# Kernel tuning notes

Measured on AMD Instinct MI355X. Metric: run time of the kernel, lower is better.

The kernel has to match this reference:

```python
import jax, jax.numpy as jnp
import numpy as np

B, T, C, H = 8, 1024, 768, 12
HD = C // H  # 64

def setup_inputs() -> dict:
    key = jax.random.key(0)
    ks = jax.random.split(key, 5)
    s = 0.02
    return {
        "x": jax.random.normal(ks[0], (B, T, C), dtype=jnp.float32),
        "w_attn": jax.random.normal(ks[1], (C, 3 * C), dtype=jnp.float32) * s,
        "b_attn": jnp.zeros((3 * C,), dtype=jnp.float32),
        "w_proj": jax.random.normal(ks[2], (C, C), dtype=jnp.float32) * s,
        "b_proj": jnp.zeros((C,), dtype=jnp.float32),
    }

def reference(x, w_attn, b_attn, w_proj, b_proj):
    Bx, Tx, Cx = x.shape
    qkv = x @ w_attn + b_attn                      # [B,T,3C]
    q, k, v = jnp.split(qkv, 3, axis=-1)
    # [B,H,T,hd]
    q = q.reshape(Bx, Tx, H, HD).transpose(0, 2, 1, 3)
    k = k.reshape(Bx, Tx, H, HD).transpose(0, 2, 1, 3)
    v = v.reshape(Bx, Tx, H, HD).transpose(0, 2, 1, 3)
    scale = 1.0 / jnp.sqrt(jnp.asarray(HD, dtype=x.dtype))
    scores = jnp.einsum('bhqd,bhkd->bhqk', q, k) * scale  # [B,H,T,T]
    causal = jnp.tril(jnp.ones((Tx, Tx), dtype=bool))
    scores = jnp.where(causal, scores, jnp.asarray(-jnp.inf, dtype=x.dtype))
    weights = jax.nn.softmax(scores, axis=-1)
    y = jnp.einsum('bhqk,bhkd->bhqd', weights, v)  # [B,H,T,hd]
    y = y.transpose(0, 2, 1, 3).reshape(Bx, Tx, Cx)
    return y @ w_proj + b_proj
```

## Files before the change

kernel.cpp:

```cpp
#include <hip/hip_runtime.h>
#include <cstdint>
#include <cstddef>

#define B_  8
#define T_  1024
#define C_  768
#define H_  12
#define HD_ 64
#define K3_ 2304

typedef unsigned short u16;
typedef __attribute__((ext_vector_type(8))) short bf16x8;
typedef __attribute__((ext_vector_type(4))) float f32x4;

#define MFMA __builtin_amdgcn_mfma_f32_16x16x32_bf16

__device__ __forceinline__ u16 f2bf(float f) {
    unsigned u = __builtin_bit_cast(unsigned, f);
    u += 0x7fffu + ((u >> 16) & 1u);
    return (u16)(u >> 16);
}

__device__ __forceinline__ unsigned pk2bf(float a, float b) {
    unsigned ua = __builtin_bit_cast(unsigned, a) + 0x8000u;
    unsigned ub = __builtin_bit_cast(unsigned, b) + 0x8000u;
    return (ua >> 16) | (ub & 0xffff0000u);
}

#define GLL16(gp, lp) __builtin_amdgcn_global_load_lds( \
    (__attribute__((address_space(1))) unsigned int*)(gp), \
    (__attribute__((address_space(3))) unsigned int*)(lp), 16, 0, 0)

__device__ __forceinline__ void tcvt_tile(const float* __restrict__ in, u16* __restrict__ out,
                                          int R, int Cc, int bx, int by, int tid, float* tile ) {
    int bc = bx * 32, br = by * 32;
    int tx = tid & 31, ty = tid >> 5;
    #pragma unroll
    for (int kk = 0; kk < 32; kk += 8)
        tile[(ty + kk) * 33 + tx] = in[(size_t)(br + ty + kk) * Cc + bc + tx];
    __syncthreads();
    #pragma unroll
    for (int kk = 0; kk < 32; kk += 8)
        out[(size_t)(bc + ty + kk) * R + br + tx] = f2bf(tile[tx * 33 + ty + kk]);
}

__global__ void prep(const float* __restrict__ x, u16* __restrict__ xb,
                     const float* __restrict__ wa, u16* __restrict__ wat,
                     const float* __restrict__ wp, u16* __restrict__ wpt) {
    __shared__ float tile[32 * 33];
    int bid = blockIdx.x, tid = threadIdx.x;
    if (bid < 6144) {
        int i = bid * 256 + tid;
        float4 v = ((const float4*)x)[i];
        ushort4 o;
        o.x = f2bf(v.x); o.y = f2bf(v.y); o.z = f2bf(v.z); o.w = f2bf(v.w);
        ((ushort4*)xb)[i] = o;
    } else if (bid < 6144 + 1728) {
        int b = bid - 6144;
        tcvt_tile(wa, wat, C_, K3_, b % 72, b / 72, tid, tile);
    } else {
        int b = bid - 7872;
        tcvt_tile(wp, wpt, C_, C_, b % 24, b / 24, tid, tile);
    }
}

__launch_bounds__(256)
__global__ void gemm_qkv(const u16* __restrict__ A, const u16* __restrict__ Bt,
                         const float* __restrict__ bias,
                         u16* __restrict__ q, u16* __restrict__ k, u16* __restrict__ v) {
    const int K = C_;
    __shared__ __align__(16) u16 SM[16896];
    u16 (*As)[64] = (u16(*)[64])SM;
    u16 (*Bs)[64] = (u16(*)[64])(SM + 8192);
    u16 (*Cs)[132] = (u16(*)[132])SM;
    int tid = threadIdx.x;
    int id = blockIdx.x;
    int xcd = id & 7, jj = id >> 3;
    int m0 = (xcd * 8 + (jj & 7)) * 128;
    int n0 = (jj >> 3) * 128;
    int lane = tid & 63, wv = tid >> 6;
    int wm = (wv >> 1) * 64, wn = (wv & 1) * 64;
    int r16 = lane & 15, quad = lane >> 4;

    f32x4 acc[4][4] = {};
    int srow = tid >> 3;
    int gblk = (tid & 7) ^ (srow & 7);
    const u16* Ag = A  + (size_t)(m0 + srow) * K + gblk * 8;
    const u16* Bg = Bt + (size_t)(n0 + srow) * K + gblk * 8;
    u16* Al = SM + tid * 8;
    u16* Bl = SM + 8192 + tid * 8;
    int sw = r16 & 7;

    for (int kt = 0; kt < K; kt += 64) {
        #pragma unroll
        for (int s = 0; s < 4; s++) {
            GLL16(Ag + (size_t)(s * 32) * K + kt, Al + s * 2048);
            GLL16(Bg + (size_t)(s * 32) * K + kt, Bl + s * 2048);
        }
        __syncthreads();
        #pragma unroll
        for (int kk = 0; kk < 2; kk++) {
            bf16x8 af[4], bfr[4];
            #pragma unroll
            for (int i = 0; i < 4; i++) af[i]  = *(const bf16x8*)&As[wm + i * 16 + r16][((kk * 4 + quad) ^ sw) * 8];
            #pragma unroll
            for (int j = 0; j < 4; j++) bfr[j] = *(const bf16x8*)&Bs[wn + j * 16 + r16][((kk * 4 + quad) ^ sw) * 8];
            #pragma unroll
            for (int i = 0; i < 4; i++)
                #pragma unroll
                for (int j = 0; j < 4; j++)
                    acc[i][j] = MFMA(af[i], bfr[j], acc[i][j], 0, 0, 0);
        }
        __syncthreads();
    }

    int sec = n0 / C_;
    int cc0 = n0 - sec * C_;
    int b = m0 >> 10, t0 = m0 & 1023;

    if (sec == 2) {
        #pragma unroll
        for (int i = 0; i < 4; i++) {
            #pragma unroll
            for (int j = 0; j < 4; j++) {
                int cc = cc0 + wn + j * 16 + r16;
                float bv = bias[2 * C_ + cc];
                int h = cc >> 6, hd = cc & 63;
                int t = t0 + wm + i * 16 + quad * 4;
                ushort4 ov;
                ov.x = f2bf(acc[i][j][0] + bv); ov.y = f2bf(acc[i][j][1] + bv);
                ov.z = f2bf(acc[i][j][2] + bv); ov.w = f2bf(acc[i][j][3] + bv);
                *(ushort4*)(v + (((size_t)b * H_ + h) * HD_ + hd) * T_ + t) = ov;
            }
        }
    } else {
        float scale = (sec == 0) ? 0.125f : 1.0f;
        u16* dst = (sec == 0) ? q : k;
        #pragma unroll
        for (int i = 0; i < 4; i++)
            #pragma unroll
            for (int j = 0; j < 4; j++) {
                int col = wn + j * 16 + r16;
                float bv = bias[sec * C_ + cc0 + col];
                #pragma unroll
                for (int r = 0; r < 4; r++)
                    Cs[wm + i * 16 + quad * 4 + r][col] = f2bf((acc[i][j][r] + bv) * scale);
            }
        __syncthreads();
        int h0 = cc0 >> 6;
        int rsel = tid >> 4;
        int hs = (tid >> 3) & 1;
        int c8 = (tid & 7) * 8;
        #pragma unroll
        for (int p = 0; p < 8; p++) {
            int rl = p * 16 + rsel;
            uint4 val = *(const uint4*)&Cs[rl][hs * 64 + c8];
            *(uint4*)(dst + (((size_t)b * H_ + h0 + hs) * T_ + t0 + rl) * HD_ + c8) = val;
        }
    }
}

__launch_bounds__(256)
__global__ void gemm_proj(const u16* __restrict__ A, const u16* __restrict__ Bt,
                          const float* __restrict__ bias, float* __restrict__ out) {
    const int K = C_, N = C_;
    __shared__ __align__(16) u16 SM[16384];
    u16 (*As)[64] = (u16(*)[64])SM;
    u16 (*Bs)[64] = (u16(*)[64])(SM + 8192);
    int tid = threadIdx.x;
    int id = blockIdx.x;
    int xcd = id & 7, jj = id >> 3;
    int m0 = (xcd * 8 + (jj & 7)) * 128;
    int n0 = (jj >> 3) * 128;
    int lane = tid & 63, wv = tid >> 6;
    int wm = (wv >> 1) * 64, wn = (wv & 1) * 64;
    int r16 = lane & 15, quad = lane >> 4;

    f32x4 acc[4][4] = {};
    int srow = tid >> 3;
    int gblk = (tid & 7) ^ (srow & 7);
    const u16* Ag = A  + (size_t)(m0 + srow) * K + gblk * 8;
    const u16* Bg = Bt + (size_t)(n0 + srow) * K + gblk * 8;
    u16* Al = SM + tid * 8;
    u16* Bl = SM + 8192 + tid * 8;
    int sw = r16 & 7;

    for (int kt = 0; kt < K; kt += 64) {
        #pragma unroll
        for (int s = 0; s < 4; s++) {
            GLL16(Ag + (size_t)(s * 32) * K + kt, Al + s * 2048);
            GLL16(Bg + (size_t)(s * 32) * K + kt, Bl + s * 2048);
        }
        __syncthreads();
        #pragma unroll
        for (int kk = 0; kk < 2; kk++) {
            bf16x8 af[4], bfr[4];
            #pragma unroll
            for (int i = 0; i < 4; i++) af[i]  = *(const bf16x8*)&As[wm + i * 16 + r16][((kk * 4 + quad) ^ sw) * 8];
            #pragma unroll
            for (int j = 0; j < 4; j++) bfr[j] = *(const bf16x8*)&Bs[wn + j * 16 + r16][((kk * 4 + quad) ^ sw) * 8];
            #pragma unroll
            for (int i = 0; i < 4; i++)
                #pragma unroll
                for (int j = 0; j < 4; j++)
                    acc[i][j] = MFMA(af[i], bfr[j], acc[i][j], 0, 0, 0);
        }
        __syncthreads();
    }

    #pragma unroll
    for (int i = 0; i < 4; i++) {
        #pragma unroll
        for (int j = 0; j < 4; j++) {
            int gn = n0 + wn + j * 16 + r16;
            float bv = bias[gn];
            #pragma unroll
            for (int r = 0; r < 4; r++) {
                int gm = m0 + wm + i * 16 + quad * 4 + r;
                out[(size_t)gm * N + gn] = acc[i][j][r] + bv;
            }
        }
    }
}

__launch_bounds__(256, 2)
__global__ void attn(const u16* __restrict__ q, const u16* __restrict__ k,
                     const u16* __restrict__ v, u16* __restrict__ y) {
    __shared__ __align__(16) u16 Kb[2][64][64];
    __shared__ __align__(16) u16 Vb[2][64][64];
    __shared__ __align__(16) u16 P[4][2][16][72];
    int tid = threadIdx.x, lane = tid & 63, w = tid >> 6;
    int r16 = lane & 15, quad = lane >> 4;
    int id = blockIdx.x;
    int bh = id % 96;
    int bi = id / 96;
    int b = bh / H_, h = bh - b * H_;
    int x = bi * 4 + w;
    int t_lo = x, t_hi = 63 - x;
    int qb_lo = t_lo * 16, qb_hi = t_hi * 16;
    const u16* qh = q + (size_t)bh * T_ * HD_;
    const u16* kh = k + (size_t)bh * T_ * HD_;
    const u16* vh = v + (size_t)bh * HD_ * T_;

    bf16x8 ql0 = *(const bf16x8*)(qh + (size_t)(qb_lo + r16) * HD_ + quad * 8);
    bf16x8 ql1 = *(const bf16x8*)(qh + (size_t)(qb_lo + r16) * HD_ + 32 + quad * 8);
    bf16x8 qh0 = *(const bf16x8*)(qh + (size_t)(qb_hi + r16) * HD_ + quad * 8);
    bf16x8 qh1 = *(const bf16x8*)(qh + (size_t)(qb_hi + r16) * HD_ + 32 + quad * 8);

    f32x4 oL[4] = {}, oH[4] = {};
    float lL = 0.f, lH = 0.f;
    int qyL = qb_lo + r16, qyH = qb_hi + r16;
    int ilo_last = bi;
    int n64 = __builtin_amdgcn_readfirstlane(16 - bi);

    int srow = lane >> 3;
    int scb  = (lane & 7) ^ srow;
    const u16* kst = kh + (size_t)(w * 16 + srow) * HD_ + scb * 8;
    const u16* vst = vh + (size_t)(w * 16 + srow) * T_ + scb * 8;
    int swz = (r16 & 7);

    {
        #pragma unroll
        for (int s2 = 0; s2 < 2; s2++) {
            GLL16(kst + (size_t)(s2 * 8) * HD_, &Kb[0][w * 16 + s2 * 8][0] + lane * 8);
            GLL16(vst + (size_t)(s2 * 8) * T_,  &Vb[0][w * 16 + s2 * 8][0] + lane * 8);
        }
    }
    __syncthreads();

    for (int it = 0; it < n64; ++it) {
        int kv0 = it * 64;
        int buf = it & 1;
        bool lo_on = (it <= ilo_last);
        if (it + 1 < n64) {
            int kvn = kv0 + 64;
            #pragma unroll
            for (int s2 = 0; s2 < 2; s2++) {
                GLL16(kst + (size_t)(kvn + s2 * 8) * HD_, &Kb[buf ^ 1][w * 16 + s2 * 8][0] + lane * 8);
                GLL16(vst + (size_t)(s2 * 8) * T_ + kvn,  &Vb[buf ^ 1][w * 16 + s2 * 8][0] + lane * 8);
            }
        }
        bf16x8 kf[4][2];
        #pragma unroll
        for (int n = 0; n < 4; n++)
            #pragma unroll
            for (int c = 0; c < 2; c++)
                kf[n][c] = *(const bf16x8*)&Kb[buf][n * 16 + r16][((c * 4 + quad) ^ swz) * 8];
        f32x4 sH[4] = {};
        #pragma unroll
        for (int n = 0; n < 4; n++) {
            sH[n] = MFMA(kf[n][0], qh0, sH[n], 0, 0, 0);
            sH[n] = MFMA(kf[n][1], qh1, sH[n], 0, 0, 0);
        }
        if (it == n64 - 1) {
            #pragma unroll
            for (int n = 0; n < 4; n++)
                #pragma unroll
                for (int r = 0; r < 4; r++)
                    if (kv0 + n * 16 + quad * 4 + r > qyH) sH[n][r] = -1e30f;
        }
        #pragma unroll
        for (int n = 0; n < 4; n++) {
            float p0 = __expf(sH[n][0]);
            float p1 = __expf(sH[n][1]);
            float p2 = __expf(sH[n][2]);
            float p3 = __expf(sH[n][3]);
            lH += (p0 + p1) + (p2 + p3);
            uint2 pd; pd.x = pk2bf(p0, p1); pd.y = pk2bf(p2, p3);
            *(uint2*)&P[w][1][r16][n * 16 + quad * 4] = pd;
        }
        if (lo_on) {
            f32x4 sL[4] = {};
            #pragma unroll
            for (int n = 0; n < 4; n++) {
                sL[n] = MFMA(kf[n][0], ql0, sL[n], 0, 0, 0);
                sL[n] = MFMA(kf[n][1], ql1, sL[n], 0, 0, 0);
            }
            if (it == ilo_last) {
                #pragma unroll
                for (int n = 0; n < 4; n++)
                    #pragma unroll
                    for (int r = 0; r < 4; r++)
                        if (kv0 + n * 16 + quad * 4 + r > qyL) sL[n][r] = -1e30f;
            }
            #pragma unroll
            for (int n = 0; n < 4; n++) {
                float p0 = __expf(sL[n][0]);
                float p1 = __expf(sL[n][1]);
                float p2 = __expf(sL[n][2]);
                float p3 = __expf(sL[n][3]);
                lL += (p0 + p1) + (p2 + p3);
                uint2 pd; pd.x = pk2bf(p0, p1); pd.y = pk2bf(p2, p3);
                *(uint2*)&P[w][0][r16][n * 16 + quad * 4] = pd;
            }
        }
        bf16x8 vf[4][2];
        #pragma unroll
        for (int j = 0; j < 4; j++)
            #pragma unroll
            for (int c = 0; c < 2; c++)
                vf[j][c] = *(const bf16x8*)&Vb[buf][j * 16 + r16][((c * 4 + quad) ^ swz) * 8];
        #pragma unroll
        for (int c = 0; c < 2; c++) {
            bf16x8 pfH = *(const bf16x8*)&P[w][1][r16][c * 32 + quad * 8];
            #pragma unroll
            for (int j = 0; j < 4; j++)
                oH[j] = MFMA(vf[j][c], pfH, oH[j], 0, 0, 0);
        }
        if (lo_on) {
            #pragma unroll
            for (int c = 0; c < 2; c++) {
                bf16x8 pfL = *(const bf16x8*)&P[w][0][r16][c * 32 + quad * 8];
                #pragma unroll
                for (int j = 0; j < 4; j++)
                    oL[j] = MFMA(vf[j][c], pfL, oL[j], 0, 0, 0);
            }
        }
        __syncthreads();
    }

    lH += __shfl_xor(lH, 16, 64);
    lH += __shfl_xor(lH, 32, 64);
    lL += __shfl_xor(lL, 16, 64);
    lL += __shfl_xor(lL, 32, 64);
    float invH = 1.f / lH, invL = 1.f / lL;
    int tqH = qb_hi + r16, tqL = qb_lo + r16;
    #pragma unroll
    for (int j = 0; j < 4; j++) {
        ushort4 ovH, ovL;
        ovH.x = f2bf(oH[j][0] * invH); ovH.y = f2bf(oH[j][1] * invH);
        ovH.z = f2bf(oH[j][2] * invH); ovH.w = f2bf(oH[j][3] * invH);
        ovL.x = f2bf(oL[j][0] * invL); ovL.y = f2bf(oL[j][1] * invL);
        ovL.z = f2bf(oL[j][2] * invL); ovL.w = f2bf(oL[j][3] * invL);
        *(ushort4*)(y + ((size_t)b * T_ + tqH) * C_ + h * 64 + j * 16 + quad * 4) = ovH;
        *(ushort4*)(y + ((size_t)b * T_ + tqL) * C_ + h * 64 + j * 16 + quad * 4) = ovL;
    }
}

extern "C" void kernel_launch(void* const* d_in, const int* in_sizes, int n_in,
                              void* d_out, int out_size, void* d_ws, size_t ws_size,
                              hipStream_t stream) {
    const float* x      = (const float*)d_in[0];
    const float* w_attn = (const float*)d_in[1];
    const float* b_attn = (const float*)d_in[2];
    const float* w_proj = (const float*)d_in[3];
    const float* b_proj = (const float*)d_in[4];
    float* out = (float*)d_out;

    char* ws = (char*)d_ws;
    size_t off = 0;
    auto alloc = [&](size_t bytes) {
        void* p = ws + off;
        off += (bytes + 255) & ~(size_t)255;
        return p;
    };
    const size_t M = (size_t)B_ * T_;
    u16* x_bf = (u16*)alloc(M * C_ * 2);
    u16* wat  = (u16*)alloc((size_t)K3_ * C_ * 2);
    u16* wpt  = (u16*)alloc((size_t)C_ * C_ * 2);
    u16* qb   = (u16*)alloc((size_t)B_ * H_ * T_ * HD_ * 2);
    u16* kb   = (u16*)alloc((size_t)B_ * H_ * T_ * HD_ * 2);
    u16* vb   = (u16*)alloc((size_t)B_ * H_ * T_ * HD_ * 2);
    u16* yb   = (u16*)alloc(M * C_ * 2);

    prep<<<6144 + 1728 + 576, 256, 0, stream>>>(x, x_bf, w_attn, wat, w_proj, wpt);
    gemm_qkv<<<8 * 144, 256, 0, stream>>>(x_bf, wat, b_attn, qb, kb, vb);
    attn<<<8 * 96, 256, 0, stream>>>(qb, kb, vb, yb);
    gemm_proj<<<8 * 48, 256, 0, stream>>>(yb, wpt, b_proj, out);
}
```

Measured before the change: 176.2 us.

## Triple-buffer LDS with K=32 stages and async prefetch in both GEMMs

Replaces the single-buffered K=64 tile loop in the QKV and projection GEMMs with a three-stage ring of K=32 LDS buffers. Global-to-LDS loads are issued two stages ahead and guarded by explicit vmcnt waits and one barrier per stage, instead of two __syncthreads per iteration. It also raises MFMA wave priority during the compute burst. The aim is to hide global load latency behind MFMA work, at the cost of more LDS per block (48KB), which may cut occupancy.

```diff
diff --git a/kernel.cpp b/kernel.cpp
--- a/kernel.cpp
+++ b/kernel.cpp
@@ -8,6 +8,7 @@
 #define H_  12
 #define HD_ 64
 #define K3_ 2304
+#define NT_ 24
 
 typedef unsigned short u16;
 typedef __attribute__((ext_vector_type(8))) short bf16x8;
@@ -64,14 +65,38 @@
     }
 }
 
+
+#define STG(Ag, Bg, Ls, ktv, b) { \
+    _Pragma("unroll") \
+    for (int s_ = 0; s_ < 2; s_++) { \
+        GLL16(Ag + (size_t)(s_ * 64) * C_ + (ktv) * 32, Ls + (b) * 8192 + s_ * 2048); \
+        GLL16(Bg + (size_t)(s_ * 64) * C_ + (ktv) * 32, Ls + (b) * 8192 + 4096 + s_ * 2048); \
+    } }
+
+#define RDMM(SMp, b) { \
+    const u16* as_ = SMp + (b) * 8192; \
+    bf16x8 af[4], bfr[4]; \
+    _Pragma("unroll") \
+    for (int i = 0; i < 4; i++) af[i]  = *(const bf16x8*)&as_[(wm + i * 16 + r16) * 32 + ((quad ^ sw) * 8)]; \
+    _Pragma("unroll") \
+    for (int j = 0; j < 4; j++) bfr[j] = *(const bf16x8*)&as_[4096 + (wn + j * 16 + r16) * 32 + ((quad ^ sw) * 8)]; \
+    __builtin_amdgcn_s_setprio(1); \
+    _Pragma("unroll") \
+    for (int i = 0; i < 4; i++) \
+        _Pragma("unroll") \
+        for (int j = 0; j < 4; j++) \
+            acc[i][j] = MFMA(af[i], bfr[j], acc[i][j], 0, 0, 0); \
+    __builtin_amdgcn_s_setprio(0); }
+
+#define VMW4 asm volatile("s_waitcnt vmcnt(4)" ::: "memory")
+#define VMW0 asm volatile("s_waitcnt vmcnt(0)" ::: "memory")
+#define BAR  __builtin_amdgcn_s_barrier()
+
 __launch_bounds__(256)
 __global__ void gemm_qkv(const u16* __restrict__ A, const u16* __restrict__ Bt,
                          const float* __restrict__ bias,
                          u16* __restrict__ q, u16* __restrict__ k, u16* __restrict__ v) {
-    const int K = C_;
-    __shared__ __align__(16) u16 SM[16896];
-    u16 (*As)[64] = (u16(*)[64])SM;
-    u16 (*Bs)[64] = (u16(*)[64])(SM + 8192);
+    __shared__ __align__(16) u16 SM[24576];
     u16 (*Cs)[132] = (u16(*)[132])SM;
     int tid = threadIdx.x;
     int id = blockIdx.x;
@@ -81,38 +106,29 @@
     int lane = tid & 63, wv = tid >> 6;
     int wm = (wv >> 1) * 64, wn = (wv & 1) * 64;
     int r16 = lane & 15, quad = lane >> 4;
+    int sw = r16 & 3;
 
     f32x4 acc[4][4] = {};
-    int srow = tid >> 3;
-    int gblk = (tid & 7) ^ (srow & 7);
-    const u16* Ag = A  + (size_t)(m0 + srow) * K + gblk * 8;
-    const u16* Bg = Bt + (size_t)(n0 + srow) * K + gblk * 8;
-    u16* Al = SM + tid * 8;
-    u16* Bl = SM + 8192 + tid * 8;
-    int sw = r16 & 7;
-
-    for (int kt = 0; kt < K; kt += 64) {
-        #pragma unroll
-        for (int s = 0; s < 4; s++) {
-            GLL16(Ag + (size_t)(s * 32) * K + kt, Al + s * 2048);
-            GLL16(Bg + (size_t)(s * 32) * K + kt, Bl + s * 2048);
-        }
-        __syncthreads();
-        #pragma unroll
-        for (int kk = 0; kk < 2; kk++) {
-            bf16x8 af[4], bfr[4];
-            #pragma unroll
-            for (int i = 0; i < 4; i++) af[i]  = *(const bf16x8*)&As[wm + i * 16 + r16][((kk * 4 + quad) ^ sw) * 8];
-            #pragma unroll
-            for (int j = 0; j < 4; j++) bfr[j] = *(const bf16x8*)&Bs[wn + j * 16 + r16][((kk * 4 + quad) ^ sw) * 8];
-            #pragma unroll
-            for (int i = 0; i < 4; i++)
-                #pragma unroll
-                for (int j = 0; j < 4; j++)
-                    acc[i][j] = MFMA(af[i], bfr[j], acc[i][j], 0, 0, 0);
-        }
-        __syncthreads();
-    }
+    int sr = wv * 16 + (lane >> 2);
+    int scb = (lane & 3) ^ (sr & 3);
+    const u16* Ag = A  + (size_t)(m0 + sr) * C_ + scb * 8;
+    const u16* Bg = Bt + (size_t)(n0 + sr) * C_ + scb * 8;
+    u16* Ls = SM + wv * 512 + lane * 8;
+
+    STG(Ag, Bg, Ls, 0, 0); STG(Ag, Bg, Ls, 1, 1);
+    VMW4; BAR;
+
+    for (int o = 0; o < 7; ++o) {
+        int kt = o * 3;
+        STG(Ag, Bg, Ls, kt + 2, 2); RDMM(SM, 0); VMW4; BAR;
+        STG(Ag, Bg, Ls, kt + 3, 0); RDMM(SM, 1); VMW4; BAR;
+        STG(Ag, Bg, Ls, kt + 4, 1); RDMM(SM, 2); VMW4; BAR;
+    }
+    STG(Ag, Bg, Ls, 23, 2); RDMM(SM, 0); VMW4; BAR;
+    RDMM(SM, 1); VMW0; BAR;
+    RDMM(SM, 2);
+
+    __syncthreads();
 
     int sec = n0 / C_;
     int cc0 = n0 - sec * C_;
@@ -163,10 +179,8 @@
 __launch_bounds__(256)
 __global__ void gemm_proj(const u16* __restrict__ A, const u16* __restrict__ Bt,
                           const float* __restrict__ bias, float* __restrict__ out) {
-    const int K = C_, N = C_;
-    __shared__ __align__(16) u16 SM[16384];
-    u16 (*As)[64] = (u16(*)[64])SM;
-    u16 (*Bs)[64] = (u16(*)[64])(SM + 8192);
+    const int N = C_;
+    __shared__ __align__(16) u16 SM[24576];
     int tid = threadIdx.x;
     int id = blockIdx.x;
     int xcd = id & 7, jj = id >> 3;
@@ -175,38 +189,27 @@
     int lane = tid & 63, wv = tid >> 6;
     int wm = (wv >> 1) * 64, wn = (wv & 1) * 64;
     int r16 = lane & 15, quad = lane >> 4;
+    int sw = r16 & 3;
 
     f32x4 acc[4][4] = {};
-    int srow = tid >> 3;
-    int gblk = (tid & 7) ^ (srow & 7);
-    const u16* Ag = A  + (size_t)(m0 + srow) * K + gblk * 8;
-    const u16* Bg = Bt + (size_t)(n0 + srow) * K + gblk * 8;
-    u16* Al = SM + tid * 8;
-    u16* Bl = SM + 8192 + tid * 8;
-    int sw = r16 & 7;
-
-    for (int kt = 0; kt < K; kt += 64) {
-        #pragma unroll
-        for (int s = 0; s < 4; s++) {
-            GLL16(Ag + (size_t)(s * 32) * K + kt, Al + s * 2048);
-            GLL16(Bg + (size_t)(s * 32) * K + kt, Bl + s * 2048);
-        }
-        __syncthreads();
-        #pragma unroll
-        for (int kk = 0; kk < 2; kk++) {
-            bf16x8 af[4], bfr[4];
-            #pragma unroll
-            for (int i = 0; i < 4; i++) af[i]  = *(const bf16x8*)&As[wm + i * 16 + r16][((kk * 4 + quad) ^ sw) * 8];
-            #pragma unroll
-            for (int j = 0; j < 4; j++) bfr[j] = *(const bf16x8*)&Bs[wn + j * 16 + r16][((kk * 4 + quad) ^ sw) * 8];
-            #pragma unroll
-            for (int i = 0; i < 4; i++)
-                #pragma unroll
-                for (int j = 0; j < 4; j++)
-                    acc[i][j] = MFMA(af[i], bfr[j], acc[i][j], 0, 0, 0);
-        }
-        __syncthreads();
-    }
+    int sr = wv * 16 + (lane >> 2);
+    int scb = (lane & 3) ^ (sr & 3);
+    const u16* Ag = A  + (size_t)(m0 + sr) * C_ + scb * 8;
+    const u16* Bg = Bt + (size_t)(n0 + sr) * C_ + scb * 8;
+    u16* Ls = SM + wv * 512 + lane * 8;
+
+    STG(Ag, Bg, Ls, 0, 0); STG(Ag, Bg, Ls, 1, 1);
+    VMW4; BAR;
+
+    for (int o = 0; o < 7; ++o) {
+        int kt = o * 3;
+        STG(Ag, Bg, Ls, kt + 2, 2); RDMM(SM, 0); VMW4; BAR;
+        STG(Ag, Bg, Ls, kt + 3, 0); RDMM(SM, 1); VMW4; BAR;
+        STG(Ag, Bg, Ls, kt + 4, 1); RDMM(SM, 2); VMW4; BAR;
+    }
+    STG(Ag, Bg, Ls, 23, 2); RDMM(SM, 0); VMW4; BAR;
+    RDMM(SM, 1); VMW0; BAR;
+    RDMM(SM, 2);
 
     #pragma unroll
     for (int i = 0; i < 4; i++) {
```

Measured after the change: 174.4 us. No clear change (-1.0%).

## Pipeline GEMMs with triple-buffered LDS and 128x256 tiles on 512 threads

Applied to the files above, without the earlier changes.

Both GEMM kernels now share a helper that triple-buffers A/B tiles in LDS. It issues global-to-LDS loads for the next K-slices while the current slice runs MFMAs, with partial vmcnt waits and raised priority around the MFMA bursts. Tiles grow from 128x128 to 128x256 with 8 waves per block, and the QKV epilogue stages through LDS in two halves. The aim is to hide global load latency and cut per-iteration barrier stalls. The cost is much more LDS per block (144KB), which lowers occupancy, and fewer blocks, which worsens wave quantization for the projection GEMM.

```diff
diff --git a/kernel.cpp b/kernel.cpp
--- a/kernel.cpp
+++ b/kernel.cpp
@@ -64,55 +64,94 @@
     }
 }
 
-__launch_bounds__(256)
+#define VMW6 asm volatile("s_waitcnt vmcnt(6)" ::: "memory")
+#define VMW0 asm volatile("s_waitcnt vmcnt(0)" ::: "memory")
+#define BAR  __builtin_amdgcn_s_barrier()
+
+__device__ __forceinline__ void gemm_pipe(const u16* __restrict__ A, const u16* __restrict__ Bt,
+                                          int m0, int n0, u16* SM, f32x4 (&acc)[4][4]) {
+    const int K = C_;
+    int tid = threadIdx.x;
+    int lane = tid & 63, wv = tid >> 6;
+    int wr = wv >> 2, wc = wv & 3;
+    int r16 = lane & 15, quad = lane >> 4;
+    int sw = r16 & 7;
+    int x0 = (quad ^ sw) * 8;
+    int x1 = ((4 + quad) ^ sw) * 8;
+    int arow = (wr * 64 + r16) * 64;
+    int brow = (wc * 64 + r16) * 64;
+    int tr = tid >> 3;
+    int tb = (tid & 7) ^ (tr & 7);
+    const u16* Ag = A  + (size_t)(m0 + tr) * K + tb * 8;
+    const u16* Bg = Bt + (size_t)(n0 + tr) * K + tb * 8;
+    u16* SLa = SM + tid * 8;
+    u16* SLb = SM + 24576 + tid * 8;
+    const u16* SMB = SM + 24576;
+
+#define STG_A(ss, kO, u)  GLL16(Ag + (size_t)(u) * 64 * K + (kO), SLa + (ss) * 8192 + (u) * 4096)
+#define STG_B(ss, kO, u)  GLL16(Bg + (size_t)(u) * 64 * K + (kO), SLb + (ss) * 16384 + (u) * 4096)
+#define STG_H0(ss, kO) { STG_A(ss, kO, 0); STG_A(ss, kO, 1); STG_B(ss, kO, 0); }
+#define STG_H1(ss, kO) { STG_B(ss, kO, 1); STG_B(ss, kO, 2); STG_B(ss, kO, 3); }
+#define RD(rs, XC) { \
+    const u16* Ar_ = SM  + (rs) * 8192  + arow; \
+    const u16* Br_ = SMB + (rs) * 16384 + brow; \
+    _Pragma("unroll") for (int i_ = 0; i_ < 4; i_++) af[i_] = *(const bf16x8*)&Ar_[i_ * 1024 + (XC)]; \
+    _Pragma("unroll") for (int j_ = 0; j_ < 4; j_++) bb[j_] = *(const bf16x8*)&Br_[j_ * 1024 + (XC)]; }
+#define MM() { \
+    __builtin_amdgcn_s_setprio(1); \
+    _Pragma("unroll") for (int i_ = 0; i_ < 4; i_++) \
+    _Pragma("unroll") for (int j_ = 0; j_ < 4; j_++) \
+        acc[i_][j_] = MFMA(af[i_], bb[j_], acc[i_][j_], 0, 0, 0); \
+    __builtin_amdgcn_s_setprio(0); }
+
+    STG_H0(0, 0);  STG_H1(0, 0);
+    STG_H0(1, 64); STG_H1(1, 64);
+    VMW6; BAR;
+
+    int sa = 0, sb = 1, sc = 2;
+    int kS = 128;
+    for (int it = 0; it < 5; ++it) {
+        bf16x8 af[4], bb[4];
+        RD(sa, x0); STG_H0(sc, kS);            BAR; MM(); BAR;
+        RD(sa, x1); STG_H1(sc, kS);      VMW6; BAR; MM(); BAR;
+        RD(sb, x0); STG_H0(sa, kS + 64);       BAR; MM(); BAR;
+        RD(sb, x1); STG_H1(sa, kS + 64); VMW6; BAR; MM(); BAR;
+        int t_ = sa; sa = sc; sc = sb; sb = t_;
+        kS += 128;
+    }
+    {
+        bf16x8 af[4], bb[4];
+        RD(sa, x0); MM();
+        RD(sa, x1); MM();
+        VMW0; BAR;
+        RD(sb, x0); MM();
+        RD(sb, x1); MM();
+    }
+#undef STG_A
+#undef STG_B
+#undef STG_H0
+#undef STG_H1
+#undef RD
+#undef MM
+}
+
+__launch_bounds__(512)
 __global__ void gemm_qkv(const u16* __restrict__ A, const u16* __restrict__ Bt,
                          const float* __restrict__ bias,
                          u16* __restrict__ q, u16* __restrict__ k, u16* __restrict__ v) {
-    const int K = C_;
-    __shared__ __align__(16) u16 SM[16896];
-    u16 (*As)[64] = (u16(*)[64])SM;
-    u16 (*Bs)[64] = (u16(*)[64])(SM + 8192);
-    u16 (*Cs)[132] = (u16(*)[132])SM;
+    __shared__ __align__(16) u16 SM[73728];
+    int id = blockIdx.x;
+    int xcd = id & 7, j = id >> 3;
+    int m0 = (xcd * 8 + (j & 7)) * 128;
+    int n0 = (j >> 3) * 256;
+    f32x4 acc[4][4] = {};
+    gemm_pipe(A, Bt, m0, n0, SM, acc);
+
     int tid = threadIdx.x;
-    int id = blockIdx.x;
-    int xcd = id & 7, jj = id >> 3;
-    int m0 = (xcd * 8 + (jj & 7)) * 128;
-    int n0 = (jj >> 3) * 128;
     int lane = tid & 63, wv = tid >> 6;
-    int wm = (wv >> 1) * 64, wn = (wv & 1) * 64;
+    int wr = wv >> 2, wc = wv & 3;
     int r16 = lane & 15, quad = lane >> 4;
-
-    f32x4 acc[4][4] = {};
-    int srow = tid >> 3;
-    int gblk = (tid & 7) ^ (srow & 7);
-    const u16* Ag = A  + (size_t)(m0 + srow) * K + gblk * 8;
-    const u16* Bg = Bt + (size_t)(n0 + srow) * K + gblk * 8;
-    u16* Al = SM + tid * 8;
-    u16* Bl = SM + 8192 + tid * 8;
-    int sw = r16 & 7;
-
-    for (int kt = 0; kt < K; kt += 64) {
-        #pragma unroll
-        for (int s = 0; s < 4; s++) {
-            GLL16(Ag + (size_t)(s * 32) * K + kt, Al + s * 2048);
-            GLL16(Bg + (size_t)(s * 32) * K + kt, Bl + s * 2048);
-        }
-        __syncthreads();
-        #pragma unroll
-        for (int kk = 0; kk < 2; kk++) {
-            bf16x8 af[4], bfr[4];
-            #pragma unroll
-            for (int i = 0; i < 4; i++) af[i]  = *(const bf16x8*)&As[wm + i * 16 + r16][((kk * 4 + quad) ^ sw) * 8];
-            #pragma unroll
-            for (int j = 0; j < 4; j++) bfr[j] = *(const bf16x8*)&Bs[wn + j * 16 + r16][((kk * 4 + quad) ^ sw) * 8];
-            #pragma unroll
-            for (int i = 0; i < 4; i++)
-                #pragma unroll
-                for (int j = 0; j < 4; j++)
-                    acc[i][j] = MFMA(af[i], bfr[j], acc[i][j], 0, 0, 0);
-        }
-        __syncthreads();
-    }
+    __syncthreads();
 
     int sec = n0 / C_;
     int cc0 = n0 - sec * C_;
@@ -122,102 +161,76 @@
         #pragma unroll
         for (int i = 0; i < 4; i++) {
             #pragma unroll
-            for (int j = 0; j < 4; j++) {
-                int cc = cc0 + wn + j * 16 + r16;
+            for (int jj = 0; jj < 4; jj++) {
+                int cc = cc0 + wc * 64 + jj * 16 + r16;
                 float bv = bias[2 * C_ + cc];
                 int h = cc >> 6, hd = cc & 63;
-                int t = t0 + wm + i * 16 + quad * 4;
+                int t = t0 + wr * 64 + i * 16 + quad * 4;
                 ushort4 ov;
-                ov.x = f2bf(acc[i][j][0] + bv); ov.y = f2bf(acc[i][j][1] + bv);
-                ov.z = f2bf(acc[i][j][2] + bv); ov.w = f2bf(acc[i][j][3] + bv);
+                ov.x = f2bf(acc[i][jj][0] + bv); ov.y = f2bf(acc[i][jj][1] + bv);
+                ov.z = f2bf(acc[i][jj][2] + bv); ov.w = f2bf(acc[i][jj][3] + bv);
                 *(ushort4*)(v + (((size_t)b * H_ + h) * HD_ + hd) * T_ + t) = ov;
             }
         }
     } else {
         float scale = (sec == 0) ? 0.125f : 1.0f;
         u16* dst = (sec == 0) ? q : k;
-        #pragma unroll
-        for (int i = 0; i < 4; i++)
-            #pragma unroll
-            for (int j = 0; j < 4; j++) {
-                int col = wn + j * 16 + r16;
-                float bv = bias[sec * C_ + cc0 + col];
+        u16 (*Cs)[136] = (u16(*)[136])SM;
+        #pragma unroll
+        for (int half = 0; half < 2; half++) {
+            if ((wc >> 1) == half) {
                 #pragma unroll
-                for (int r = 0; r < 4; r++)
-                    Cs[wm + i * 16 + quad * 4 + r][col] = f2bf((acc[i][j][r] + bv) * scale);
-            }
-        __syncthreads();
-        int h0 = cc0 >> 6;
-        int rsel = tid >> 4;
-        int hs = (tid >> 3) & 1;
-        int c8 = (tid & 7) * 8;
-        #pragma unroll
-        for (int p = 0; p < 8; p++) {
-            int rl = p * 16 + rsel;
-            uint4 val = *(const uint4*)&Cs[rl][hs * 64 + c8];
-            *(uint4*)(dst + (((size_t)b * H_ + h0 + hs) * T_ + t0 + rl) * HD_ + c8) = val;
-        }
-    }
-}
-
-__launch_bounds__(256)
+                for (int i = 0; i < 4; i++)
+                    #pragma unroll
+                    for (int jj = 0; jj < 4; jj++) {
+                        int col = (wc & 1) * 64 + jj * 16 + r16;
+                        float bv = bias[sec * C_ + cc0 + half * 128 + col];
+                        #pragma unroll
+                        for (int r = 0; r < 4; r++)
+                            Cs[wr * 64 + i * 16 + quad * 4 + r][col] = f2bf((acc[i][jj][r] + bv) * scale);
+                    }
+            }
+            __syncthreads();
+            int rsel = tid >> 4;
+            int ch = tid & 15;
+            int hh = (cc0 + half * 128 + ch * 8) >> 6;
+            int hd0 = (ch & 7) * 8;
+            #pragma unroll
+            for (int p = 0; p < 4; p++) {
+                int rl = p * 32 + rsel;
+                uint4 val = *(const uint4*)&Cs[rl][ch * 8];
+                *(uint4*)(dst + (((size_t)b * H_ + hh) * T_ + t0 + rl) * HD_ + hd0) = val;
+            }
+            __syncthreads();
+        }
+    }
+}
+
+__launch_bounds__(512)
 __global__ void gemm_proj(const u16* __restrict__ A, const u16* __restrict__ Bt,
                           const float* __restrict__ bias, float* __restrict__ out) {
-    const int K = C_, N = C_;
-    __shared__ __align__(16) u16 SM[16384];
-    u16 (*As)[64] = (u16(*)[64])SM;
-    u16 (*Bs)[64] = (u16(*)[64])(SM + 8192);
+    __shared__ __align__(16) u16 SM[73728];
+    int id = blockIdx.x;
+    int xcd = id & 7, j = id >> 3;
+    int m0 = (xcd * 8 + (j & 7)) * 128;
+    int n0 = (j >> 3) * 256;
+    f32x4 acc[4][4] = {};
+    gemm_pipe(A, Bt, m0, n0, SM, acc);
+
     int tid = threadIdx.x;
-    int id = blockIdx.x;
-    int xcd = id & 7, jj = id >> 3;
-    int m0 = (xcd * 8 + (jj & 7)) * 128;
-    int n0 = (jj >> 3) * 128;
     int lane = tid & 63, wv = tid >> 6;
-    int wm = (wv >> 1) * 64, wn = (wv & 1) * 64;
+    int wr = wv >> 2, wc = wv & 3;
     int r16 = lane & 15, quad = lane >> 4;
-
-    f32x4 acc[4][4] = {};
-    int srow = tid >> 3;
-    int gblk = (tid & 7) ^ (srow & 7);
-    const u16* Ag = A  + (size_t)(m0 + srow) * K + gblk * 8;
-    const u16* Bg = Bt + (size_t)(n0 + srow) * K + gblk * 8;
-    u16* Al = SM + tid * 8;
-    u16* Bl = SM + 8192 + tid * 8;
-    int sw = r16 & 7;
-
-    for (int kt = 0; kt < K; kt += 64) {
-        #pragma unroll
-        for (int s = 0; s < 4; s++) {
-            GLL16(Ag + (size_t)(s * 32) * K + kt, Al + s * 2048);
-            GLL16(Bg + (size_t)(s * 32) * K + kt, Bl + s * 2048);
-        }
-        __syncthreads();
-        #pragma unroll
-        for (int kk = 0; kk < 2; kk++) {
-            bf16x8 af[4], bfr[4];
-            #pragma unroll
-            for (int i = 0; i < 4; i++) af[i]  = *(const bf16x8*)&As[wm + i * 16 + r16][((kk * 4 + quad) ^ sw) * 8];
-            #pragma unroll
-            for (int j = 0; j < 4; j++) bfr[j] = *(const bf16x8*)&Bs[wn + j * 16 + r16][((kk * 4 + quad) ^ sw) * 8];
-            #pragma unroll
-            for (int i = 0; i < 4; i++)
-                #pragma unroll
-                for (int j = 0; j < 4; j++)
-                    acc[i][j] = MFMA(af[i], bfr[j], acc[i][j], 0, 0, 0);
-        }
-        __syncthreads();
-    }
-
     #pragma unroll
     for (int i = 0; i < 4; i++) {
         #pragma unroll
-        for (int j = 0; j < 4; j++) {
-            int gn = n0 + wn + j * 16 + r16;
+        for (int jj = 0; jj < 4; jj++) {
+            int gn = n0 + wc * 64 + jj * 16 + r16;
             float bv = bias[gn];
             #pragma unroll
             for (int r = 0; r < 4; r++) {
-                int gm = m0 + wm + i * 16 + quad * 4 + r;
-                out[(size_t)gm * N + gn] = acc[i][j][r] + bv;
+                int gm = m0 + wr * 64 + i * 16 + quad * 4 + r;
+                out[(size_t)gm * C_ + gn] = acc[i][jj][r] + bv;
             }
         }
     }
@@ -404,7 +417,7 @@
     u16* yb   = (u16*)alloc(M * C_ * 2);
 
     prep<<<6144 + 1728 + 576, 256, 0, stream>>>(x, x_bf, w_attn, wat, w_proj, wpt);
-    gemm_qkv<<<8 * 144, 256, 0, stream>>>(x_bf, wat, b_attn, qb, kb, vb);
+    gemm_qkv<<<576, 512, 0, stream>>>(x_bf, wat, b_attn, qb, kb, vb);
     attn<<<8 * 96, 256, 0, stream>>>(qb, kb, vb, yb);
-    gemm_proj<<<8 * 48, 256, 0, stream>>>(yb, wpt, b_proj, out);
-}
+    gemm_proj<<<192, 512, 0, stream>>>(yb, wpt, b_proj, out);
+}
```

New measurement: 168.7 us. 4.2% less time.
